# Optimization experiments

Hardware: AMD Instinct MI355X
Metric: run time of the kernel (lower is better)

## Reference

```python
import jax, jax.numpy as jnp
import numpy as np

T, D, H, E, V = 256, 512, 256, 256, 8192  # steps, max_ast_depth, hidden=units, emb dim, vocab


def setup_inputs() -> dict:
    key = jax.random.key(0)
    ks = jax.random.split(key, 12)
    s = 1.0 / np.sqrt(H)
    u = lambda k, shp: jax.random.uniform(k, shp, jnp.float32, -s, s)
    return {
        "nodes": jax.random.randint(ks[0], (T, D), 0, V),
        "edges": jax.random.randint(ks[1], (T, D), 0, 2).astype(bool),
        "initial_state": jax.random.normal(ks[2], (1, D, H), jnp.float32),
        "emb": jax.random.normal(ks[3], (V, E), jnp.float32) * 0.02,
        "c_Wih": u(ks[4], (3 * H, E)), "c_Whh": u(ks[5], (3 * H, H)),
        "c_bih": u(ks[6], (3 * H,)), "c_bhh": u(ks[7], (3 * H,)),
        "s_Wih": u(ks[8], (3 * H, E)), "s_Whh": u(ks[9], (3 * H, H)),
        "s_bih": u(ks[10], (3 * H,)), "s_bhh": u(ks[11], (3 * H,)),
    }


def _gru_cell(x, h, Wih, Whh, bih, bhh):
    # torch GRU cell math: gates ordered (r, z, n)
    gi = x @ Wih.T + bih           # [D, 3H]
    gh = h @ Whh.T + bhh           # [D, 3H]
    ir, iz, in_ = jnp.split(gi, 3, axis=-1)
    hr, hz, hn = jnp.split(gh, 3, axis=-1)
    r = jax.nn.sigmoid(ir + hr)
    z = jax.nn.sigmoid(iz + hz)
    n = jnp.tanh(in_ + r * hn)
    return (1.0 - z) * n + z * h   # [D, H]


def reference(nodes, edges, initial_state, emb,
              c_Wih, c_Whh, c_bih, c_bhh,
              s_Wih, s_Whh, s_bih, s_bhh):
    # Single-layer dual GRU: per step, run both GRUs on the same state and
    # route per node via the boolean edge mask (child vs sibling).
    def step(h, te):
        node_t, edge_t = te            # [D] int, [D] bool
        x = emb[node_t]                # [D, E] embedding gather
        hc = _gru_cell(x, h, c_Wih, c_Whh, c_bih, c_bhh)
        hs = _gru_cell(x, h, s_Wih, s_Whh, s_bih, s_bhh)
        h_new = jnp.where(edge_t[:, None], hc, hs)  # [D, H]
        return h_new, h_new            # output == new state for 1-layer GRU (seq_len 1)

    h_final, outs = jax.lax.scan(step, initial_state[0], (nodes, edges))
    # match torch shapes: outputs [T, D, 1, H], state [num_layers, D, H]
    return outs[:, :, None, :], h_final[None]
```

## Files before the change

kernel.cpp:

```cpp
#include <hip/hip_runtime.h>
#include <stdint.h>


#define TT   256
#define DDIM 512
#define LSTR 264

typedef float    float4v __attribute__((ext_vector_type(4)));
typedef short    short8  __attribute__((ext_vector_type(8)));
typedef uint32_t uint4v  __attribute__((ext_vector_type(4)));

__device__ __forceinline__ unsigned short f2bf(float f){
  uint32_t u = __float_as_uint(f);
  u += 0x7fffu + ((u >> 16) & 1u);
  return (unsigned short)(u >> 16);
}
__device__ __forceinline__ float bf2f(unsigned short h){
  return __uint_as_float(((uint32_t)h) << 16);
}
__device__ __forceinline__ float4v splat4(float v){ return (float4v){v, v, v, v}; }

__global__ __launch_bounds__(256, 1)
void treernn_main(const int* __restrict__ nodes,
                  const unsigned char* __restrict__ edges,
                  const unsigned char* __restrict__ hinit,
                  const unsigned char* __restrict__ emb,
                  const unsigned char* __restrict__ cWih, const unsigned char* __restrict__ cWhh,
                  const unsigned char* __restrict__ cbih, const unsigned char* __restrict__ cbhh,
                  const unsigned char* __restrict__ sWih, const unsigned char* __restrict__ sWhh,
                  const unsigned char* __restrict__ sbih, const unsigned char* __restrict__ sbhh,
                  unsigned char* __restrict__ out,
                  unsigned char* __restrict__ ws)
{
  __shared__ __align__(16) unsigned short xs[2][16 * LSTR];
  __shared__ __align__(16) unsigned short hstg[16 * LSTR];
  __shared__ float hold[16 * 33];
  __shared__ int det[8];

  const int tid  = threadIdx.x;
  const int lane = tid & 63;
  const int wv   = tid >> 6;
  const int gru  = wv >> 1;
  const int ch   = wv & 1;
  const int quad = lane >> 4;
  const int l16  = lane & 15;
  const int bid  = blockIdx.x;

  const int G    = bid >> 3;
  const int cs   = bid & 7;
  const int d0   = G * 16;
  const int colw = ch * 16 + l16;
  const int col  = cs * 32 + colw;

  if (tid < 8) det[tid] = 0;
  __syncthreads();
  {
    const unsigned short* hu = (const unsigned short*)hinit;
    int ce = 0;
    for (int i = tid; i < 4096; i += 256){
      const int e = (hu[i] >> 7) & 0xFF;
      ce += (e >= 100 && e <= 130) ? 1 : 0;
    }
    atomicAdd(&det[0], ce);
    const uint32_t* ewp = (const uint32_t*)edges;
    int b01 = 0, w01 = 0, wf = 0, hb = 0;
    for (int i = tid; i < 512; i += 256){
      const uint32_t w = ewp[i];
      w01 += (w <= 1u) ? 1 : 0;
      wf  += (w == 0u || w == 0x3F800000u) ? 1 : 0;
      const uint32_t h0 = w & 0xFFFFu, h1 = w >> 16;
      hb  += ((h0 == 0u || h0 == 0x3F80u) ? 1 : 0) + ((h1 == 0u || h1 == 0x3F80u) ? 1 : 0);
      b01 += (((w      ) & 0xFFu) <= 1u ? 1 : 0) + (((w >> 8 ) & 0xFFu) <= 1u ? 1 : 0)
           + (((w >> 16) & 0xFFu) <= 1u ? 1 : 0) + (((w >> 24)        ) <= 1u ? 1 : 0);
    }
    atomicAdd(&det[1], b01); atomicAdd(&det[2], w01);
    atomicAdd(&det[3], wf);  atomicAdd(&det[4], hb);
  }
  __syncthreads();
  const int fdt = (det[0] >= 3480) ? 1 : 0;
  int efmt;
  if      (det[2] == 512)  efmt = 1;
  else if (det[1] == 2048) efmt = 0;
  else if (det[4] == 1024) efmt = 3;
  else if (det[3] == 512)  efmt = 2;
  else                     efmt = 0;

  uint32_t*       flg = (uint32_t*)ws;
  unsigned short* xbp = (unsigned short*)(ws + 16384);

  const unsigned char* Wihp = gru ? sWih : cWih;
  const unsigned char* Whhp = gru ? sWhh : cWhh;
  const unsigned char* bihp = gru ? sbih : cbih;
  const unsigned char* bhhp = gru ? sbhh : cbhh;

  float bI[3], bH[3];
  #pragma unroll
  for (int ga = 0; ga < 3; ++ga){
    if (fdt){
      bI[ga] = bf2f(((const unsigned short*)bihp)[ga * 256 + col]);
      bH[ga] = bf2f(((const unsigned short*)bhhp)[ga * 256 + col]);
    } else {
      bI[ga] = ((const float*)bihp)[ga * 256 + col];
      bH[ga] = ((const float*)bhhp)[ga * 256 + col];
    }
  }

  short8 wI[3][8], wH[3][8];
  for (int ga = 0; ga < 3; ++ga){
    const int rw = ga * 256 + col;
    for (int kc = 0; kc < 8; ++kc){
      const int ke = kc * 32 + quad * 8;
      if (fdt){
        wI[ga][kc] = *(const short8*)((const unsigned short*)Wihp + (size_t)rw * 256 + ke);
        wH[ga][kc] = *(const short8*)((const unsigned short*)Whhp + (size_t)rw * 256 + ke);
      } else {
        const float* pI = (const float*)Wihp + (size_t)rw * 256 + ke;
        const float* pH = (const float*)Whhp + (size_t)rw * 256 + ke;
        short8 va, vb;
        #pragma unroll
        for (int j = 0; j < 8; ++j){ va[j] = (short)f2bf(pI[j]); vb[j] = (short)f2bf(pH[j]); }
        wI[ga][kc] = va; wH[ga][kc] = vb;
      }
    }
  }

  {
    const int row = tid >> 4, cb = (tid & 15) * 16;
    const int nd = nodes[d0 + row];
    unsigned short* xdst = &xs[0][row * LSTR + cb];
    unsigned short* hdst = &hstg[row * LSTR + cb];
    if (fdt){
      const unsigned short* sx = (const unsigned short*)emb   + (size_t)nd * 256 + cb;
      const unsigned short* sh = (const unsigned short*)hinit + (size_t)(d0 + row) * 256 + cb;
      *(uint4v*)xdst       = *(const uint4v*)sx;
      *(uint4v*)(xdst + 8) = *(const uint4v*)(sx + 8);
      *(uint4v*)hdst       = *(const uint4v*)sh;
      *(uint4v*)(hdst + 8) = *(const uint4v*)(sh + 8);
    } else {
      const float* sx = (const float*)emb   + (size_t)nd * 256 + cb;
      const float* sh = (const float*)hinit + (size_t)(d0 + row) * 256 + cb;
      short8 v0, v1, w0, w1;
      #pragma unroll
      for (int j = 0; j < 8; ++j){
        v0[j] = (short)f2bf(sx[j]); v1[j] = (short)f2bf(sx[8 + j]);
        w0[j] = (short)f2bf(sh[j]); w1[j] = (short)f2bf(sh[8 + j]);
      }
      *(short8*)xdst = v0; *(short8*)(xdst + 8) = v1;
      *(short8*)hdst = w0; *(short8*)(hdst + 8) = w1;
    }
    if (gru == 0){
      #pragma unroll
      for (int r = 0; r < 4; ++r){
        const size_t si = (size_t)(d0 + quad * 4 + r) * 256 + col;
        hold[(quad * 4 + r) * 33 + colw] =
            fdt ? bf2f(((const unsigned short*)hinit)[si]) : ((const float*)hinit)[si];
      }
    }
  }
  int ef[4];
  {
    const int base = d0 + quad * 4;
    if (efmt == 0){      for (int r = 0; r < 4; ++r) ef[r] = edges[base + r] != 0; }
    else if (efmt == 1){ for (int r = 0; r < 4; ++r) ef[r] = ((const int*)edges)[base + r] != 0; }
    else if (efmt == 3){ for (int r = 0; r < 4; ++r) ef[r] = ((const unsigned short*)edges)[base + r] != 0; }
    else {               for (int r = 0; r < 4; ++r) ef[r] = ((const float*)edges)[base + r] != 0.0f; }
  }
  __syncthreads();

  const int grow = tid >> 4;
  const int gsub = tid & 15;
  uint32_t* flgG = flg + G * 32;

  uint32_t sPk[4] = {0, 0, 0, 0};
  float    sCd[4] = {0, 0, 0, 0};
  int      sMn[4] = {0, 0, 0, 0};

  for (int t = 0; t < TT; ++t){
    if (t > 0){
      #pragma unroll
      for (int r = 0; r < 4; ++r){
        const int row = quad * 4 + r;
        if (fdt){
          if (sMn[r] && !(lane & 1)){
            unsigned short* o16 = (unsigned short*)out;
            *(uint32_t*)(o16 + (size_t)(t - 1) * 131072 + (size_t)(d0 + row) * 256 + col) = sPk[r];
          }
        } else {
          if (sMn[r]){
            float* o32 = (float*)out;
            o32[(size_t)(t - 1) * 131072 + (size_t)(d0 + row) * 256 + col] = sCd[r];
          }
        }
      }
    }

    float4v aI[3];
    #pragma unroll
    for (int ga = 0; ga < 3; ++ga) aI[ga] = splat4(bI[ga]);
    {
      const unsigned short* xc = xs[t & 1];
      #pragma unroll
      for (int kc = 0; kc < 8; ++kc){
        short8 a = *(const short8*)&xc[l16 * LSTR + kc * 32 + quad * 8];
        #pragma unroll
        for (int ga = 0; ga < 3; ++ga)
          aI[ga] = __builtin_amdgcn_mfma_f32_16x16x32_bf16(a, wI[ga][kc], aI[ga], 0, 0, 0);
      }
    }

    float hold4[4];
    #pragma unroll
    for (int r = 0; r < 4; ++r) hold4[r] = hold[(quad * 4 + r) * 33 + colw];

    if (t > 0){
      const uint32_t target = (uint32_t)t;
      const uint32_t* fp = flgG + (lane & 31);
      uint32_t fv = __hip_atomic_load(fp, __ATOMIC_RELAXED, __HIP_MEMORY_SCOPE_AGENT);
      int guard = 0;
      while (__ballot(fv < target) != 0ull){
        __builtin_amdgcn_s_sleep(1);
        fv = __hip_atomic_load(fp, __ATOMIC_RELAXED, __HIP_MEMORY_SCOPE_AGENT);
        if (++guard > (1 << 17)) break;
      }
      __atomic_signal_fence(__ATOMIC_SEQ_CST);
      const uint64_t* src = (const uint64_t*)(xbp + ((size_t)(t & 1) * 512 + d0 + grow) * 256
                                                  + gsub * 16);
      uint64_t a0 = __hip_atomic_load(src + 0, __ATOMIC_RELAXED, __HIP_MEMORY_SCOPE_AGENT);
      uint64_t a1 = __hip_atomic_load(src + 1, __ATOMIC_RELAXED, __HIP_MEMORY_SCOPE_AGENT);
      uint64_t a2 = __hip_atomic_load(src + 2, __ATOMIC_RELAXED, __HIP_MEMORY_SCOPE_AGENT);
      uint64_t a3 = __hip_atomic_load(src + 3, __ATOMIC_RELAXED, __HIP_MEMORY_SCOPE_AGENT);
      unsigned short* dst = &hstg[grow * LSTR + gsub * 16];
      *(uint64_t*)(dst + 0)  = a0;
      *(uint64_t*)(dst + 4)  = a1;
      *(uint64_t*)(dst + 8)  = a2;
      *(uint64_t*)(dst + 12) = a3;
    }
    __syncthreads();

    float4v aH[3];
    #pragma unroll
    for (int ga = 0; ga < 3; ++ga) aH[ga] = splat4(bH[ga]);
    #pragma unroll
    for (int kc = 0; kc < 8; ++kc){
      short8 a = *(const short8*)&hstg[l16 * LSTR + kc * 32 + quad * 8];
      #pragma unroll
      for (int ga = 0; ga < 3; ++ga)
        aH[ga] = __builtin_amdgcn_mfma_f32_16x16x32_bf16(a, wH[ga][kc], aH[ga], 0, 0, 0);
    }

    float cand[4]; int mine[4];
    #pragma unroll
    for (int r = 0; r < 4; ++r){
      const float pr = aI[0][r] + aH[0][r];
      const float pz = aI[1][r] + aH[1][r];
      const float R  = 1.0f / (1.0f + exp2f(-1.4426950408889634f * pr));
      const float Z  = 1.0f / (1.0f + exp2f(-1.4426950408889634f * pz));
      float ag = aI[2][r] + R * aH[2][r];
      ag = fminf(30.0f, fmaxf(-30.0f, ag));
      const float ex = exp2f(-2.8853900817779268f * ag);
      const float N  = (1.0f - ex) / (1.0f + ex);
      cand[r] = N + Z * (hold4[r] - N);
      mine[r] = ((ef[r] != 0) == (gru == 0)) ? 1 : 0;
    }

    const int buf = (t + 1) & 1;
    #pragma unroll
    for (int r = 0; r < 4; ++r){
      const int row = quad * 4 + r;
      if (mine[r]) hold[row * 33 + colw] = cand[r];
      const uint32_t bb = (uint32_t)f2bf(cand[r]);
      const uint32_t ob = (uint32_t)__shfl_xor((int)bb, 1, 64);
      const uint32_t pk = bb | (ob << 16);
      sPk[r] = pk; sCd[r] = cand[r]; sMn[r] = mine[r];
      if (t < TT - 1 && mine[r] && !(lane & 1)){
        uint32_t* xp = (uint32_t*)&xbp[((size_t)buf * 512 + d0 + row) * 256 + col];
        __hip_atomic_store(xp, pk, __ATOMIC_RELAXED, __HIP_MEMORY_SCOPE_AGENT);
      }
    }

    if (t < TT - 1){
      __atomic_signal_fence(__ATOMIC_SEQ_CST);
      __builtin_amdgcn_s_waitcnt(0x0F70);
      __atomic_signal_fence(__ATOMIC_SEQ_CST);
      if (lane == 0)
        __hip_atomic_store(flgG + cs * 4 + wv, (uint32_t)(t + 1),
                           __ATOMIC_RELAXED, __HIP_MEMORY_SCOPE_AGENT);

      {
        const int row = tid >> 4, cb = (tid & 15) * 16;
        const int nd = nodes[(t + 1) * DDIM + d0 + row];
        unsigned short* dst = &xs[buf][row * LSTR + cb];
        if (fdt){
          const unsigned short* s = (const unsigned short*)emb + (size_t)nd * 256 + cb;
          uint4v r0 = *(const uint4v*)s;
          uint4v r1 = *(const uint4v*)(s + 8);
          *(uint4v*)dst       = r0;
          *(uint4v*)(dst + 8) = r1;
        } else {
          const float* s = (const float*)emb + (size_t)nd * 256 + cb;
          short8 v0, v1;
          #pragma unroll
          for (int j = 0; j < 8; ++j){ v0[j] = (short)f2bf(s[j]); v1[j] = (short)f2bf(s[8 + j]); }
          *(short8*)dst       = v0;
          *(short8*)(dst + 8) = v1;
        }
        const int eb = (t + 1) * DDIM + d0 + quad * 4;
        if (efmt == 0){      for (int r2 = 0; r2 < 4; ++r2) ef[r2] = edges[eb + r2] != 0; }
        else if (efmt == 1){ for (int r2 = 0; r2 < 4; ++r2) ef[r2] = ((const int*)edges)[eb + r2] != 0; }
        else if (efmt == 3){ for (int r2 = 0; r2 < 4; ++r2) ef[r2] = ((const unsigned short*)edges)[eb + r2] != 0; }
        else {               for (int r2 = 0; r2 < 4; ++r2) ef[r2] = ((const float*)edges)[eb + r2] != 0.0f; }
      }
    }

    __syncthreads();
  }

  #pragma unroll
  for (int r = 0; r < 4; ++r){
    const int row = quad * 4 + r;
    if (fdt){
      if (sMn[r] && !(lane & 1)){
        unsigned short* o16 = (unsigned short*)out;
        *(uint32_t*)(o16 + (size_t)255 * 131072 + (size_t)(d0 + row) * 256 + col) = sPk[r];
        *(uint32_t*)(o16 + (size_t)256 * 131072 + (size_t)(d0 + row) * 256 + col) = sPk[r];
      }
    } else {
      if (sMn[r]){
        float* o32 = (float*)out;
        o32[(size_t)255 * 131072 + (size_t)(d0 + row) * 256 + col] = sCd[r];
        o32[(size_t)256 * 131072 + (size_t)(d0 + row) * 256 + col] = sCd[r];
      }
    }
  }
}

extern "C" void kernel_launch(void* const* d_in, const int* in_sizes, int n_in,
                              void* d_out, int out_size, void* d_ws, size_t ws_size,
                              hipStream_t stream)
{
  const int*           nodes = (const int*)d_in[0];
  const unsigned char* edges = (const unsigned char*)d_in[1];
  const unsigned char* hinit = (const unsigned char*)d_in[2];
  const unsigned char* emb   = (const unsigned char*)d_in[3];
  const unsigned char* cWih  = (const unsigned char*)d_in[4];
  const unsigned char* cWhh  = (const unsigned char*)d_in[5];
  const unsigned char* cbih  = (const unsigned char*)d_in[6];
  const unsigned char* cbhh  = (const unsigned char*)d_in[7];
  const unsigned char* sWih  = (const unsigned char*)d_in[8];
  const unsigned char* sWhh  = (const unsigned char*)d_in[9];
  const unsigned char* sbih  = (const unsigned char*)d_in[10];
  const unsigned char* sbhh  = (const unsigned char*)d_in[11];
  (void)in_sizes; (void)n_in; (void)out_size; (void)ws_size;

  hipMemsetAsync(d_ws, 0, 8192, stream);

  treernn_main<<<dim3(256), dim3(256), 0, stream>>>(
      nodes, edges, hinit, emb, cWih, cWhh, cbih, cbhh, sWih, sWhh, sbih, sbhh,
      (unsigned char*)d_out, (unsigned char*)d_ws);
}
```

Baseline: 1.258 ms.

## Load MFMA fragments directly from global, precompute input gates, drop per-step barriers

Removes the LDS staging buffers for embeddings and hidden state; each lane now loads its MFMA A-fragments straight from global memory (embedding rows and the cross-block exchange buffer). The input-gate GEMM for step t+1 is computed right after publishing the step-t flag, off the critical path of the next wait. The hold buffer is double-buffered so both __syncthreads per step can be removed. Risks include less-coalesced fragment loads, a full waitcnt(0) before the flag store, and a much smaller spin guard (1024) that could break out early and read stale state.

```diff
diff --git a/kernel.cpp b/kernel.cpp
--- a/kernel.cpp
+++ b/kernel.cpp
@@ -4,7 +4,7 @@
 
 #define TT   256
 #define DDIM 512
-#define LSTR 264
+#define GUARD_ITERS 1024
 
 typedef float    float4v __attribute__((ext_vector_type(4)));
 typedef short    short8  __attribute__((ext_vector_type(8)));
@@ -19,6 +19,8 @@
   return __uint_as_float(((uint32_t)h) << 16);
 }
 __device__ __forceinline__ float4v splat4(float v){ return (float4v){v, v, v, v}; }
+
+union FragU { short8 v; uint64_t q[2]; };
 
 __global__ __launch_bounds__(256, 1)
 void treernn_main(const int* __restrict__ nodes,
@@ -32,9 +34,7 @@
                   unsigned char* __restrict__ out,
                   unsigned char* __restrict__ ws)
 {
-  __shared__ __align__(16) unsigned short xs[2][16 * LSTR];
-  __shared__ __align__(16) unsigned short hstg[16 * LSTR];
-  __shared__ float hold[16 * 33];
+  __shared__ float hold[2][16 * 33];
   __shared__ int det[8];
 
   const int tid  = threadIdx.x;
@@ -51,6 +51,7 @@
   const int d0   = G * 16;
   const int colw = ch * 16 + l16;
   const int col  = cs * 32 + colw;
+  const int myrow = d0 + l16;
 
   if (tid < 8) det[tid] = 0;
   __syncthreads();
@@ -124,39 +125,67 @@
     }
   }
 
+  short8 frag[8];
+  float4v gi[3];
+
   {
-    const int row = tid >> 4, cb = (tid & 15) * 16;
-    const int nd = nodes[d0 + row];
-    unsigned short* xdst = &xs[0][row * LSTR + cb];
-    unsigned short* hdst = &hstg[row * LSTR + cb];
+    const int nd = nodes[myrow];
     if (fdt){
-      const unsigned short* sx = (const unsigned short*)emb   + (size_t)nd * 256 + cb;
-      const unsigned short* sh = (const unsigned short*)hinit + (size_t)(d0 + row) * 256 + cb;
-      *(uint4v*)xdst       = *(const uint4v*)sx;
-      *(uint4v*)(xdst + 8) = *(const uint4v*)(sx + 8);
-      *(uint4v*)hdst       = *(const uint4v*)sh;
-      *(uint4v*)(hdst + 8) = *(const uint4v*)(sh + 8);
+      const unsigned short* p16 = (const unsigned short*)emb + (size_t)nd * 256 + quad * 8;
+      #pragma unroll
+      for (int kc = 0; kc < 8; ++kc) frag[kc] = *(const short8*)(p16 + kc * 32);
     } else {
-      const float* sx = (const float*)emb   + (size_t)nd * 256 + cb;
-      const float* sh = (const float*)hinit + (size_t)(d0 + row) * 256 + cb;
-      short8 v0, v1, w0, w1;
-      #pragma unroll
-      for (int j = 0; j < 8; ++j){
-        v0[j] = (short)f2bf(sx[j]); v1[j] = (short)f2bf(sx[8 + j]);
-        w0[j] = (short)f2bf(sh[j]); w1[j] = (short)f2bf(sh[8 + j]);
-      }
-      *(short8*)xdst = v0; *(short8*)(xdst + 8) = v1;
-      *(short8*)hdst = w0; *(short8*)(hdst + 8) = w1;
-    }
-    if (gru == 0){
-      #pragma unroll
-      for (int r = 0; r < 4; ++r){
-        const size_t si = (size_t)(d0 + quad * 4 + r) * 256 + col;
-        hold[(quad * 4 + r) * 33 + colw] =
-            fdt ? bf2f(((const unsigned short*)hinit)[si]) : ((const float*)hinit)[si];
-      }
-    }
-  }
+      const float* p32 = (const float*)emb + (size_t)nd * 256 + quad * 8;
+      #pragma unroll
+      for (int kc = 0; kc < 8; ++kc){
+        uint4v a = *(const uint4v*)(p32 + kc * 32);
+        uint4v b = *(const uint4v*)(p32 + kc * 32 + 4);
+        short8 v;
+        #pragma unroll
+        for (int j = 0; j < 4; ++j){ v[j] = (short)f2bf(__uint_as_float(a[j]));
+                                     v[4 + j] = (short)f2bf(__uint_as_float(b[j])); }
+        frag[kc] = v;
+      }
+    }
+    #pragma unroll
+    for (int ga = 0; ga < 3; ++ga) gi[ga] = splat4(bI[ga]);
+    #pragma unroll
+    for (int kc = 0; kc < 8; ++kc){
+      #pragma unroll
+      for (int ga = 0; ga < 3; ++ga)
+        gi[ga] = __builtin_amdgcn_mfma_f32_16x16x32_bf16(frag[kc], wI[ga][kc], gi[ga], 0, 0, 0);
+    }
+  }
+
+  {
+    if (fdt){
+      const unsigned short* p16 = (const unsigned short*)hinit + (size_t)myrow * 256 + quad * 8;
+      #pragma unroll
+      for (int kc = 0; kc < 8; ++kc) frag[kc] = *(const short8*)(p16 + kc * 32);
+    } else {
+      const float* p32 = (const float*)hinit + (size_t)myrow * 256 + quad * 8;
+      #pragma unroll
+      for (int kc = 0; kc < 8; ++kc){
+        uint4v a = *(const uint4v*)(p32 + kc * 32);
+        uint4v b = *(const uint4v*)(p32 + kc * 32 + 4);
+        short8 v;
+        #pragma unroll
+        for (int j = 0; j < 4; ++j){ v[j] = (short)f2bf(__uint_as_float(a[j]));
+                                     v[4 + j] = (short)f2bf(__uint_as_float(b[j])); }
+        frag[kc] = v;
+      }
+    }
+  }
+
+  if (gru == 0){
+    #pragma unroll
+    for (int r = 0; r < 4; ++r){
+      const size_t si = (size_t)(d0 + quad * 4 + r) * 256 + col;
+      hold[0][(quad * 4 + r) * 33 + colw] =
+          fdt ? bf2f(((const unsigned short*)hinit)[si]) : ((const float*)hinit)[si];
+    }
+  }
+
   int ef[4];
   {
     const int base = d0 + quad * 4;
@@ -167,10 +196,7 @@
   }
   __syncthreads();
 
-  const int grow = tid >> 4;
-  const int gsub = tid & 15;
   uint32_t* flgG = flg + G * 32;
-
   uint32_t sPk[4] = {0, 0, 0, 0};
   float    sCd[4] = {0, 0, 0, 0};
   int      sMn[4] = {0, 0, 0, 0};
@@ -194,24 +220,6 @@
       }
     }
 
-    float4v aI[3];
-    #pragma unroll
-    for (int ga = 0; ga < 3; ++ga) aI[ga] = splat4(bI[ga]);
-    {
-      const unsigned short* xc = xs[t & 1];
-      #pragma unroll
-      for (int kc = 0; kc < 8; ++kc){
-        short8 a = *(const short8*)&xc[l16 * LSTR + kc * 32 + quad * 8];
-        #pragma unroll
-        for (int ga = 0; ga < 3; ++ga)
-          aI[ga] = __builtin_amdgcn_mfma_f32_16x16x32_bf16(a, wI[ga][kc], aI[ga], 0, 0, 0);
-      }
-    }
-
-    float hold4[4];
-    #pragma unroll
-    for (int r = 0; r < 4; ++r) hold4[r] = hold[(quad * 4 + r) * 33 + colw];
-
     if (t > 0){
       const uint32_t target = (uint32_t)t;
       const uint32_t* fp = flgG + (lane & 31);
@@ -220,42 +228,42 @@
       while (__ballot(fv < target) != 0ull){
         __builtin_amdgcn_s_sleep(1);
         fv = __hip_atomic_load(fp, __ATOMIC_RELAXED, __HIP_MEMORY_SCOPE_AGENT);
-        if (++guard > (1 << 17)) break;
+        if (++guard > GUARD_ITERS) break;
       }
       __atomic_signal_fence(__ATOMIC_SEQ_CST);
-      const uint64_t* src = (const uint64_t*)(xbp + ((size_t)(t & 1) * 512 + d0 + grow) * 256
-                                                  + gsub * 16);
-      uint64_t a0 = __hip_atomic_load(src + 0, __ATOMIC_RELAXED, __HIP_MEMORY_SCOPE_AGENT);
-      uint64_t a1 = __hip_atomic_load(src + 1, __ATOMIC_RELAXED, __HIP_MEMORY_SCOPE_AGENT);
-      uint64_t a2 = __hip_atomic_load(src + 2, __ATOMIC_RELAXED, __HIP_MEMORY_SCOPE_AGENT);
-      uint64_t a3 = __hip_atomic_load(src + 3, __ATOMIC_RELAXED, __HIP_MEMORY_SCOPE_AGENT);
-      unsigned short* dst = &hstg[grow * LSTR + gsub * 16];
-      *(uint64_t*)(dst + 0)  = a0;
-      *(uint64_t*)(dst + 4)  = a1;
-      *(uint64_t*)(dst + 8)  = a2;
-      *(uint64_t*)(dst + 12) = a3;
-    }
-    __syncthreads();
+      const uint64_t* srcq = (const uint64_t*)xbp
+          + ((((size_t)(t & 1) * 512 + myrow) * 256) >> 2) + quad * 2;
+      #pragma unroll
+      for (int kc = 0; kc < 8; ++kc){
+        FragU f;
+        f.q[0] = __hip_atomic_load(srcq + kc * 8 + 0, __ATOMIC_RELAXED, __HIP_MEMORY_SCOPE_AGENT);
+        f.q[1] = __hip_atomic_load(srcq + kc * 8 + 1, __ATOMIC_RELAXED, __HIP_MEMORY_SCOPE_AGENT);
+        frag[kc] = f.v;
+      }
+    }
+
+    float hold4[4];
+    #pragma unroll
+    for (int r = 0; r < 4; ++r) hold4[r] = hold[t & 1][(quad * 4 + r) * 33 + colw];
 
     float4v aH[3];
     #pragma unroll
     for (int ga = 0; ga < 3; ++ga) aH[ga] = splat4(bH[ga]);
     #pragma unroll
     for (int kc = 0; kc < 8; ++kc){
-      short8 a = *(const short8*)&hstg[l16 * LSTR + kc * 32 + quad * 8];
       #pragma unroll
       for (int ga = 0; ga < 3; ++ga)
-        aH[ga] = __builtin_amdgcn_mfma_f32_16x16x32_bf16(a, wH[ga][kc], aH[ga], 0, 0, 0);
+        aH[ga] = __builtin_amdgcn_mfma_f32_16x16x32_bf16(frag[kc], wH[ga][kc], aH[ga], 0, 0, 0);
     }
 
     float cand[4]; int mine[4];
     #pragma unroll
     for (int r = 0; r < 4; ++r){
-      const float pr = aI[0][r] + aH[0][r];
-      const float pz = aI[1][r] + aH[1][r];
+      const float pr = gi[0][r] + aH[0][r];
+      const float pz = gi[1][r] + aH[1][r];
       const float R  = 1.0f / (1.0f + exp2f(-1.4426950408889634f * pr));
       const float Z  = 1.0f / (1.0f + exp2f(-1.4426950408889634f * pz));
-      float ag = aI[2][r] + R * aH[2][r];
+      float ag = gi[2][r] + R * aH[2][r];
       ag = fminf(30.0f, fmaxf(-30.0f, ag));
       const float ex = exp2f(-2.8853900817779268f * ag);
       const float N  = (1.0f - ex) / (1.0f + ex);
@@ -267,42 +275,51 @@
     #pragma unroll
     for (int r = 0; r < 4; ++r){
       const int row = quad * 4 + r;
-      if (mine[r]) hold[row * 33 + colw] = cand[r];
+      if (mine[r]) hold[buf][row * 33 + colw] = cand[r];
       const uint32_t bb = (uint32_t)f2bf(cand[r]);
       const uint32_t ob = (uint32_t)__shfl_xor((int)bb, 1, 64);
       const uint32_t pk = bb | (ob << 16);
       sPk[r] = pk; sCd[r] = cand[r]; sMn[r] = mine[r];
       if (t < TT - 1 && mine[r] && !(lane & 1)){
-        uint32_t* xp = (uint32_t*)&xbp[((size_t)buf * 512 + d0 + row) * 256 + col];
+        uint32_t* xp = (uint32_t*)xbp + ((size_t)buf * 512 + d0 + row) * 128 + (col >> 1);
         __hip_atomic_store(xp, pk, __ATOMIC_RELAXED, __HIP_MEMORY_SCOPE_AGENT);
       }
     }
 
     if (t < TT - 1){
       __atomic_signal_fence(__ATOMIC_SEQ_CST);
-      __builtin_amdgcn_s_waitcnt(0x0F70);
+      __builtin_amdgcn_s_waitcnt(0);
       __atomic_signal_fence(__ATOMIC_SEQ_CST);
       if (lane == 0)
         __hip_atomic_store(flgG + cs * 4 + wv, (uint32_t)(t + 1),
                            __ATOMIC_RELAXED, __HIP_MEMORY_SCOPE_AGENT);
 
       {
-        const int row = tid >> 4, cb = (tid & 15) * 16;
-        const int nd = nodes[(t + 1) * DDIM + d0 + row];
-        unsigned short* dst = &xs[buf][row * LSTR + cb];
+        const int nd = nodes[(t + 1) * DDIM + myrow];
         if (fdt){
-          const unsigned short* s = (const unsigned short*)emb + (size_t)nd * 256 + cb;
-          uint4v r0 = *(const uint4v*)s;
-          uint4v r1 = *(const uint4v*)(s + 8);
-          *(uint4v*)dst       = r0;
-          *(uint4v*)(dst + 8) = r1;
+          const unsigned short* p16 = (const unsigned short*)emb + (size_t)nd * 256 + quad * 8;
+          #pragma unroll
+          for (int kc = 0; kc < 8; ++kc) frag[kc] = *(const short8*)(p16 + kc * 32);
         } else {
-          const float* s = (const float*)emb + (size_t)nd * 256 + cb;
-          short8 v0, v1;
+          const float* p32 = (const float*)emb + (size_t)nd * 256 + quad * 8;
           #pragma unroll
-          for (int j = 0; j < 8; ++j){ v0[j] = (short)f2bf(s[j]); v1[j] = (short)f2bf(s[8 + j]); }
-          *(short8*)dst       = v0;
-          *(short8*)(dst + 8) = v1;
+          for (int kc = 0; kc < 8; ++kc){
+            uint4v a = *(const uint4v*)(p32 + kc * 32);
+            uint4v b = *(const uint4v*)(p32 + kc * 32 + 4);
+            short8 v;
+            #pragma unroll
+            for (int j = 0; j < 4; ++j){ v[j] = (short)f2bf(__uint_as_float(a[j]));
+                                         v[4 + j] = (short)f2bf(__uint_as_float(b[j])); }
+            frag[kc] = v;
+          }
+        }
+        #pragma unroll
+        for (int ga = 0; ga < 3; ++ga) gi[ga] = splat4(bI[ga]);
+        #pragma unroll
+        for (int kc = 0; kc < 8; ++kc){
+          #pragma unroll
+          for (int ga = 0; ga < 3; ++ga)
+            gi[ga] = __builtin_amdgcn_mfma_f32_16x16x32_bf16(frag[kc], wI[ga][kc], gi[ga], 0, 0, 0);
         }
         const int eb = (t + 1) * DDIM + d0 + quad * 4;
         if (efmt == 0){      for (int r2 = 0; r2 < 4; ++r2) ef[r2] = edges[eb + r2] != 0; }
@@ -311,8 +328,6 @@
         else {               for (int r2 = 0; r2 < 4; ++r2) ef[r2] = ((const float*)edges)[eb + r2] != 0.0f; }
       }
     }
-
-    __syncthreads();
   }
 
   #pragma unroll
```

Result: slower. 2.266 ms (+80.1%).
